# Kernel optimization log

Measured on AMD Instinct MI355X. Metric: run time of the kernel, lower is better.

Reference implementation:

```python
import jax, jax.numpy as jnp
import numpy as np

N_LAYERS = 4
N_QUBITS = 2
BATCH = 1_048_576

_I2 = jnp.eye(2, dtype=jnp.complex64)
_X2 = jnp.array([[0.0, 1.0], [1.0, 0.0]], dtype=jnp.complex64)


def _rx_batch(theta):
    """Batched RX(theta): (B,) -> (B,2,2) complex64. RX = cos(t/2) I - i sin(t/2) X."""
    c = jnp.cos(theta * 0.5)
    s = jnp.sin(theta * 0.5)
    return c[:, None, None] * _I2 - 1j * s[:, None, None] * _X2


def _rot(phi, theta, omega):
    """PennyLane Rot(phi, theta, omega) = RZ(omega) RY(theta) RZ(phi), 2x2 complex."""
    c = jnp.cos(theta * 0.5)
    s = jnp.sin(theta * 0.5)
    ep = jnp.exp(-0.5j * (phi + omega))  # e^{-i(phi+omega)/2}
    em = jnp.exp(-0.5j * (phi - omega))  # e^{-i(phi-omega)/2}
    return jnp.stack([
        jnp.stack([ep * c, -jnp.conj(em) * s]),
        jnp.stack([em * s, jnp.conj(ep) * c]),
    ]).astype(jnp.complex64)


def _quantum(inputs, weights):
    """Simulate the 2-qubit re-uploading circuit for a batch of inputs.

    inputs: (B, 2) float angles; weights: (N_LAYERS, 2, 3) float.
    State is stored as (B, 2, 2) complex64 indexed [batch, qubit0, qubit1].
    Returns (B, 2): [<Z0>, <Z1>].
    """
    B = inputs.shape[0]
    state = jnp.zeros((B, 2, 2), dtype=jnp.complex64).at[:, 0, 0].set(1.0)
    U0 = _rx_batch(inputs[:, 0])  # per-sample RX on wire 0
    U1 = _rx_batch(inputs[:, 1])  # per-sample RX on wire 1
    for l in range(N_LAYERS):
        # AngleEmbedding (default rotation='X'): RX(x0) wire0, RX(x1) wire1
        state = jnp.einsum('bij,bjk->bik', U0, state)
        state = jnp.einsum('bij,bkj->bki', U1, state)
        # StronglyEntanglingLayers, one layer: Rot on each wire (shared weights)
        R0 = _rot(weights[l, 0, 0], weights[l, 0, 1], weights[l, 0, 2])
        R1 = _rot(weights[l, 1, 0], weights[l, 1, 1], weights[l, 1, 2])
        state = jnp.einsum('ij,bjk->bik', R0, state)
        state = jnp.einsum('ij,bkj->bki', R1, state)
        # ring of CNOTs with range 1 on 2 wires: CNOT(0,1) then CNOT(1,0)
        state = jnp.stack([state[:, 0, :], state[:, 1, ::-1]], axis=1)  # CNOT(0,1)
        state = jnp.stack([state[:, :, 0], state[:, ::-1, 1]], axis=2)  # CNOT(1,0)
    p = state.real ** 2 + state.imag ** 2  # (B,2,2) probabilities
    z0 = p[:, 0, :].sum(-1) - p[:, 1, :].sum(-1)
    z1 = p[:, :, 0].sum(-1) - p[:, :, 1].sum(-1)
    return jnp.stack([z0, z1], axis=-1)


def setup_inputs() -> dict:
    key = jax.random.key(0)
    ks = jax.random.split(key, 8)
    return {
        'x': jax.random.normal(ks[0], (BATCH, 2), dtype=jnp.float32),
        'pre_w1': jax.random.normal(ks[1], (4, 2), dtype=jnp.float32) * 0.5,
        'pre_b1': jax.random.normal(ks[2], (4,), dtype=jnp.float32) * 0.1,
        'pre_w2': jax.random.normal(ks[3], (2, 4), dtype=jnp.float32) * 0.5,
        'pre_b2': jax.random.normal(ks[4], (2,), dtype=jnp.float32) * 0.1,
        'q_weights': jax.random.uniform(ks[5], (N_LAYERS, N_QUBITS, 3), dtype=jnp.float32,
                                        minval=0.0, maxval=2.0 * np.pi),
        'post_w': jax.random.normal(ks[6], (1, 2), dtype=jnp.float32) * 0.5,
        'post_b': jax.random.normal(ks[7], (1,), dtype=jnp.float32) * 0.1,
    }


def reference(x, pre_w1, pre_b1, pre_w2, pre_b2, q_weights, post_w, post_b):
    # classical pre: Linear(2->4)+Tanh, Linear(4->2)+Tanh
    h = jnp.tanh(x @ pre_w1.T + pre_b1)
    h = jnp.tanh(h @ pre_w2.T + pre_b2)
    # quantum layer: two PauliZ expectations in [-1, 1]
    q = _quantum(h, q_weights)
    q = (q + 1.0) * 0.5
    # classical post: Linear(2->1) + Sigmoid
    return jax.nn.sigmoid(q @ post_w.T + post_b)
```

## Files before the change

kernel.cpp:

```cpp
#include <hip/hip_runtime.h>


struct c2 { float re, im; };

__device__ __forceinline__ c2 cmul(c2 a, c2 b) {
    c2 r;
    r.re = fmaf(a.re, b.re, -(a.im * b.im));
    r.im = fmaf(a.re, b.im, a.im * b.re);
    return r;
}

__device__ __forceinline__ c2 cfma(c2 a, c2 b, c2 acc) {
    acc.re = fmaf(a.re, b.re, fmaf(-a.im, b.im, acc.re));
    acc.im = fmaf(a.re, b.im, fmaf(a.im, b.re, acc.im));
    return acc;
}

__device__ __forceinline__ void rx_pair(c2& u, c2& v, float c, float s) {
    c2 nu, nv;
    nu.re = fmaf(c, u.re,  s * v.im);
    nu.im = fmaf(c, u.im, -(s * v.re));
    nv.re = fmaf(c, v.re,  s * u.im);
    nv.im = fmaf(c, v.im, -(s * u.re));
    u = nu; v = nv;
}

__device__ __forceinline__ void rot_pair(c2& u, c2& v, c2 g00, c2 g01, c2 g10, c2 g11) {
    c2 nu = cmul(g00, u); nu = cfma(g01, v, nu);
    c2 nv = cmul(g10, u); nv = cfma(g11, v, nv);
    u = nu; v = nv;
}

__device__ __forceinline__ float ftanh(float v) {
    float e = __expf(2.0f * v);
    return __fdividef(e - 1.0f, e + 1.0f);
}

__global__ __launch_bounds__(256) void hybrid_kernel(
    const float* __restrict__ x,
    const float* __restrict__ pre_w1,
    const float* __restrict__ pre_b1,
    const float* __restrict__ pre_w2,
    const float* __restrict__ pre_b2,
    const float* __restrict__ qw,
    const float* __restrict__ post_w,
    const float* __restrict__ post_b,
    float* __restrict__ out,
    int nbatch)
{
    __shared__ float Rs[4][2][8];
    int tid = threadIdx.x;
    if (tid < 8) {
        int l = tid >> 1, w = tid & 1;
        const float* p = qw + (l * 2 + w) * 3;
        float phi = p[0], th = p[1], om = p[2];
        float c  = cosf(0.5f * th), s = sinf(0.5f * th);
        float a  = 0.5f * (phi + om), b = 0.5f * (phi - om);
        float ca = cosf(a), sa = sinf(a);
        float cb = cosf(b), sb = sinf(b);
        float* r = Rs[l][w];
        r[0] =  c * ca;  r[1] = -c * sa;
        r[2] = -s * cb;  r[3] = -s * sb;
        r[4] =  s * cb;  r[5] = -s * sb;
        r[6] =  c * ca;  r[7] =  c * sa;
    }
    __syncthreads();

    float w1[8], b1[4], w2[8], b2[2];
#pragma unroll
    for (int i = 0; i < 8; i++) w1[i] = pre_w1[i];
#pragma unroll
    for (int i = 0; i < 4; i++) b1[i] = pre_b1[i];
#pragma unroll
    for (int i = 0; i < 8; i++) w2[i] = pre_w2[i];
#pragma unroll
    for (int i = 0; i < 2; i++) b2[i] = pre_b2[i];
    float pw0 = post_w[0], pw1 = post_w[1], pb = post_b[0];

    int base = (blockIdx.x * blockDim.x + threadIdx.x) * 2;
    if (base >= nbatch) return;

    float4 xin = *reinterpret_cast<const float4*>(x + 2 * (long long)base);
    float xs0[2] = { xin.x, xin.z };
    float xs1[2] = { xin.y, xin.w };
    float res[2];

#pragma unroll
    for (int t = 0; t < 2; t++) {
        float x0 = xs0[t], x1 = xs1[t];

        float h0 = ftanh(fmaf(w1[0], x0, fmaf(w1[1], x1, b1[0])));
        float h1 = ftanh(fmaf(w1[2], x0, fmaf(w1[3], x1, b1[1])));
        float h2 = ftanh(fmaf(w1[4], x0, fmaf(w1[5], x1, b1[2])));
        float h3 = ftanh(fmaf(w1[6], x0, fmaf(w1[7], x1, b1[3])));
        float g0 = ftanh(fmaf(w2[0], h0, fmaf(w2[1], h1, fmaf(w2[2], h2, fmaf(w2[3], h3, b2[0])))));
        float g1 = ftanh(fmaf(w2[4], h0, fmaf(w2[5], h1, fmaf(w2[6], h2, fmaf(w2[7], h3, b2[1])))));

        float cs0 = __cosf(0.5f * g0), sn0 = __sinf(0.5f * g0);
        float cs1 = __cosf(0.5f * g1), sn1 = __sinf(0.5f * g1);

        c2 s00 = {1.0f, 0.0f}, s01 = {0.0f, 0.0f};
        c2 s10 = {0.0f, 0.0f}, s11 = {0.0f, 0.0f};

#pragma unroll
        for (int l = 0; l < 4; l++) {
            rx_pair(s00, s10, cs0, sn0);
            rx_pair(s01, s11, cs0, sn0);
            rx_pair(s00, s01, cs1, sn1);
            rx_pair(s10, s11, cs1, sn1);
            {
                const float* r = Rs[l][0];
                c2 g00 = {r[0], r[1]}, g01 = {r[2], r[3]};
                c2 g10 = {r[4], r[5]}, g11 = {r[6], r[7]};
                rot_pair(s00, s10, g00, g01, g10, g11);
                rot_pair(s01, s11, g00, g01, g10, g11);
            }
            {
                const float* r = Rs[l][1];
                c2 g00 = {r[0], r[1]}, g01 = {r[2], r[3]};
                c2 g10 = {r[4], r[5]}, g11 = {r[6], r[7]};
                rot_pair(s00, s01, g00, g01, g10, g11);
                rot_pair(s10, s11, g00, g01, g10, g11);
            }
            { c2 tmp = s10; s10 = s11; s11 = tmp; }
            { c2 tmp = s01; s01 = s11; s11 = tmp; }
        }

        float p00 = fmaf(s00.re, s00.re, s00.im * s00.im);
        float p01 = fmaf(s01.re, s01.re, s01.im * s01.im);
        float p10 = fmaf(s10.re, s10.re, s10.im * s10.im);
        float p11 = fmaf(s11.re, s11.re, s11.im * s11.im);
        float z0 = (p00 + p01) - (p10 + p11);
        float z1 = (p00 + p10) - (p01 + p11);

        float q0 = 0.5f * (z0 + 1.0f);
        float q1 = 0.5f * (z1 + 1.0f);
        float y  = fmaf(pw0, q0, fmaf(pw1, q1, pb));
        res[t] = __fdividef(1.0f, 1.0f + __expf(-y));
    }

    *reinterpret_cast<float2*>(out + base) = make_float2(res[0], res[1]);
}

extern "C" void kernel_launch(void* const* d_in, const int* in_sizes, int n_in,
                              void* d_out, int out_size, void* d_ws, size_t ws_size,
                              hipStream_t stream) {
    const float* x      = (const float*)d_in[0];
    const float* pre_w1 = (const float*)d_in[1];
    const float* pre_b1 = (const float*)d_in[2];
    const float* pre_w2 = (const float*)d_in[3];
    const float* pre_b2 = (const float*)d_in[4];
    const float* qw     = (const float*)d_in[5];
    const float* post_w = (const float*)d_in[6];
    const float* post_b = (const float*)d_in[7];
    float* out = (float*)d_out;

    int nbatch  = in_sizes[0] / 2;
    int threads = 256;
    int spb     = threads * 2;
    int blocks  = (nbatch + spb - 1) / spb;
    hipLaunchKernelGGL(hybrid_kernel, dim3(blocks), dim3(threads), 0, stream,
                       x, pre_w1, pre_b1, pre_w2, pre_b2, qw, post_w, post_b,
                       out, nbatch);
}
```

Baseline: 85.46 us.

## Replace per-sample circuit simulation with bilinear lookup in precomputed table

Splits the work into a table-build kernel that evaluates the quantum circuit and post layer on a 256x256 grid over the pre-activation range, and an eval kernel that runs the classical pre layers and bilinearly interpolates the table. This removes the per-sample trig and complex gate arithmetic, the main compute cost. In exchange it adds a second launch, gather loads from a 256KB table, and interpolation error relative to exact simulation.

New measurement: 78.87 us. -7.7%, faster.

```diff
diff --git a/kernel.cpp b/kernel.cpp
--- a/kernel.cpp
+++ b/kernel.cpp
@@ -1,5 +1,7 @@
 #include <hip/hip_runtime.h>
 
+
+#define TN 256
 
 struct c2 { float re, im; };
 
@@ -36,17 +38,65 @@
     return __fdividef(e - 1.0f, e + 1.0f);
 }
 
-__global__ __launch_bounds__(256) void hybrid_kernel(
-    const float* __restrict__ x,
-    const float* __restrict__ pre_w1,
-    const float* __restrict__ pre_b1,
+__device__ __forceinline__ void u_bounds(const float* w2, const float* b2,
+                                         float& B0, float& B1) {
+    B0 = fabsf(w2[0]) + fabsf(w2[1]) + fabsf(w2[2]) + fabsf(w2[3]) + fabsf(b2[0]);
+    B1 = fabsf(w2[4]) + fabsf(w2[5]) + fabsf(w2[6]) + fabsf(w2[7]) + fabsf(b2[1]);
+}
+
+__device__ __forceinline__ float circuit_y(float g0, float g1,
+                                           const float (*Rs)[2][8],
+                                           float pw0, float pw1, float pb) {
+    float cs0 = __cosf(0.5f * g0), sn0 = __sinf(0.5f * g0);
+    float cs1 = __cosf(0.5f * g1), sn1 = __sinf(0.5f * g1);
+
+    c2 s00 = {1.0f, 0.0f}, s01 = {0.0f, 0.0f};
+    c2 s10 = {0.0f, 0.0f}, s11 = {0.0f, 0.0f};
+
+#pragma unroll
+    for (int l = 0; l < 4; l++) {
+        rx_pair(s00, s10, cs0, sn0);
+        rx_pair(s01, s11, cs0, sn0);
+        rx_pair(s00, s01, cs1, sn1);
+        rx_pair(s10, s11, cs1, sn1);
+        {
+            const float* r = Rs[l][0];
+            c2 g00 = {r[0], r[1]}, g01 = {r[2], r[3]};
+            c2 g10 = {r[4], r[5]}, g11 = {r[6], r[7]};
+            rot_pair(s00, s10, g00, g01, g10, g11);
+            rot_pair(s01, s11, g00, g01, g10, g11);
+        }
+        {
+            const float* r = Rs[l][1];
+            c2 g00 = {r[0], r[1]}, g01 = {r[2], r[3]};
+            c2 g10 = {r[4], r[5]}, g11 = {r[6], r[7]};
+            rot_pair(s00, s01, g00, g01, g10, g11);
+            rot_pair(s10, s11, g00, g01, g10, g11);
+        }
+        { c2 tmp = s10; s10 = s11; s11 = tmp; }
+        { c2 tmp = s01; s01 = s11; s11 = tmp; }
+    }
+
+    float p00 = fmaf(s00.re, s00.re, s00.im * s00.im);
+    float p01 = fmaf(s01.re, s01.re, s01.im * s01.im);
+    float p10 = fmaf(s10.re, s10.re, s10.im * s10.im);
+    float p11 = fmaf(s11.re, s11.re, s11.im * s11.im);
+    float z0 = (p00 + p01) - (p10 + p11);
+    float z1 = (p00 + p10) - (p01 + p11);
+
+    float q0 = 0.5f * (z0 + 1.0f);
+    float q1 = 0.5f * (z1 + 1.0f);
+    float y  = fmaf(pw0, q0, fmaf(pw1, q1, pb));
+    return __fdividef(1.0f, 1.0f + __expf(-y));
+}
+
+__global__ __launch_bounds__(256) void build_table(
+    const float* __restrict__ qw,
     const float* __restrict__ pre_w2,
     const float* __restrict__ pre_b2,
-    const float* __restrict__ qw,
     const float* __restrict__ post_w,
     const float* __restrict__ post_b,
-    float* __restrict__ out,
-    int nbatch)
+    float* __restrict__ table)
 {
     __shared__ float Rs[4][2][8];
     int tid = threadIdx.x;
@@ -66,6 +116,31 @@
     }
     __syncthreads();
 
+    int k = blockIdx.x * 256 + tid;
+    int i = k & (TN - 1);
+    int j = k >> 8;
+
+    float B0, B1;
+    u_bounds(pre_w2, pre_b2, B0, B1);
+
+    float u0 = fmaf((2.0f * B0) / (float)(TN - 1), (float)i, -B0);
+    float u1 = fmaf((2.0f * B1) / (float)(TN - 1), (float)j, -B1);
+    float g0 = ftanh(u0);
+    float g1 = ftanh(u1);
+
+    table[k] = circuit_y(g0, g1, Rs, post_w[0], post_w[1], post_b[0]);
+}
+
+__global__ __launch_bounds__(256) void eval_kernel(
+    const float* __restrict__ x,
+    const float* __restrict__ pre_w1,
+    const float* __restrict__ pre_b1,
+    const float* __restrict__ pre_w2,
+    const float* __restrict__ pre_b2,
+    const float* __restrict__ table,
+    float* __restrict__ out,
+    int nbatch)
+{
     float w1[8], b1[4], w2[8], b2[2];
 #pragma unroll
     for (int i = 0; i < 8; i++) w1[i] = pre_w1[i];
@@ -75,7 +150,11 @@
     for (int i = 0; i < 8; i++) w2[i] = pre_w2[i];
 #pragma unroll
     for (int i = 0; i < 2; i++) b2[i] = pre_b2[i];
-    float pw0 = post_w[0], pw1 = post_w[1], pb = post_b[0];
+
+    float B0, B1;
+    u_bounds(w2, b2, B0, B1);
+    float sc0 = (float)(TN - 1) / (2.0f * B0);
+    float sc1 = (float)(TN - 1) / (2.0f * B1);
 
     int base = (blockIdx.x * blockDim.x + threadIdx.x) * 2;
     if (base >= nbatch) return;
@@ -93,50 +172,26 @@
         float h1 = ftanh(fmaf(w1[2], x0, fmaf(w1[3], x1, b1[1])));
         float h2 = ftanh(fmaf(w1[4], x0, fmaf(w1[5], x1, b1[2])));
         float h3 = ftanh(fmaf(w1[6], x0, fmaf(w1[7], x1, b1[3])));
-        float g0 = ftanh(fmaf(w2[0], h0, fmaf(w2[1], h1, fmaf(w2[2], h2, fmaf(w2[3], h3, b2[0])))));
-        float g1 = ftanh(fmaf(w2[4], h0, fmaf(w2[5], h1, fmaf(w2[6], h2, fmaf(w2[7], h3, b2[1])))));
-
-        float cs0 = __cosf(0.5f * g0), sn0 = __sinf(0.5f * g0);
-        float cs1 = __cosf(0.5f * g1), sn1 = __sinf(0.5f * g1);
-
-        c2 s00 = {1.0f, 0.0f}, s01 = {0.0f, 0.0f};
-        c2 s10 = {0.0f, 0.0f}, s11 = {0.0f, 0.0f};
-
-#pragma unroll
-        for (int l = 0; l < 4; l++) {
-            rx_pair(s00, s10, cs0, sn0);
-            rx_pair(s01, s11, cs0, sn0);
-            rx_pair(s00, s01, cs1, sn1);
-            rx_pair(s10, s11, cs1, sn1);
-            {
-                const float* r = Rs[l][0];
-                c2 g00 = {r[0], r[1]}, g01 = {r[2], r[3]};
-                c2 g10 = {r[4], r[5]}, g11 = {r[6], r[7]};
-                rot_pair(s00, s10, g00, g01, g10, g11);
-                rot_pair(s01, s11, g00, g01, g10, g11);
-            }
-            {
-                const float* r = Rs[l][1];
-                c2 g00 = {r[0], r[1]}, g01 = {r[2], r[3]};
-                c2 g10 = {r[4], r[5]}, g11 = {r[6], r[7]};
-                rot_pair(s00, s01, g00, g01, g10, g11);
-                rot_pair(s10, s11, g00, g01, g10, g11);
-            }
-            { c2 tmp = s10; s10 = s11; s11 = tmp; }
-            { c2 tmp = s01; s01 = s11; s11 = tmp; }
-        }
-
-        float p00 = fmaf(s00.re, s00.re, s00.im * s00.im);
-        float p01 = fmaf(s01.re, s01.re, s01.im * s01.im);
-        float p10 = fmaf(s10.re, s10.re, s10.im * s10.im);
-        float p11 = fmaf(s11.re, s11.re, s11.im * s11.im);
-        float z0 = (p00 + p01) - (p10 + p11);
-        float z1 = (p00 + p10) - (p01 + p11);
-
-        float q0 = 0.5f * (z0 + 1.0f);
-        float q1 = 0.5f * (z1 + 1.0f);
-        float y  = fmaf(pw0, q0, fmaf(pw1, q1, pb));
-        res[t] = __fdividef(1.0f, 1.0f + __expf(-y));
+
+        float u0 = fmaf(w2[0], h0, fmaf(w2[1], h1, fmaf(w2[2], h2, fmaf(w2[3], h3, b2[0]))));
+        float u1 = fmaf(w2[4], h0, fmaf(w2[5], h1, fmaf(w2[6], h2, fmaf(w2[7], h3, b2[1]))));
+
+        float t0 = (u0 + B0) * sc0;
+        float t1 = (u1 + B1) * sc1;
+        t0 = fminf(fmaxf(t0, 0.0f), (float)(TN - 1));
+        t1 = fminf(fmaxf(t1, 0.0f), (float)(TN - 1));
+        float i0f = fminf(floorf(t0), (float)(TN - 2));
+        float j0f = fminf(floorf(t1), (float)(TN - 2));
+        float f0 = t0 - i0f;
+        float f1 = t1 - j0f;
+        int i0 = (int)i0f;
+        int j0 = (int)j0f;
+
+        const float* p = table + j0 * TN + i0;
+        float a = p[0], b = p[1], c = p[TN], d = p[TN + 1];
+        float top = fmaf(f0, b - a, a);
+        float bot = fmaf(f0, d - c, c);
+        res[t] = fmaf(f1, bot - top, top);
     }
 
     *reinterpret_cast<float2*>(out + base) = make_float2(res[0], res[1]);
@@ -153,13 +208,16 @@
     const float* qw     = (const float*)d_in[5];
     const float* post_w = (const float*)d_in[6];
     const float* post_b = (const float*)d_in[7];
-    float* out = (float*)d_out;
+    float* out   = (float*)d_out;
+    float* table = (float*)d_ws;
+
+    hipLaunchKernelGGL(build_table, dim3((TN * TN) / 256), dim3(256), 0, stream,
+                       qw, pre_w2, pre_b2, post_w, post_b, table);
 
     int nbatch  = in_sizes[0] / 2;
     int threads = 256;
     int spb     = threads * 2;
     int blocks  = (nbatch + spb - 1) / spb;
-    hipLaunchKernelGGL(hybrid_kernel, dim3(blocks), dim3(threads), 0, stream,
-                       x, pre_w1, pre_b1, pre_w2, pre_b2, qw, post_w, post_b,
-                       out, nbatch);
-}
+    hipLaunchKernelGGL(eval_kernel, dim3(blocks), dim3(threads), 0, stream,
+                       x, pre_w1, pre_b1, pre_w2, pre_b2, table, out, nbatch);
+}
```
